# Performance work log

Hardware: AMD Instinct MI355X
Metric: run time of the kernel (lower is better)

The kernel has to match this reference:

```python
import jax, jax.numpy as jnp
import numpy as np

D_MODEL = 1024
D_HEAD = 64  # d_model / num_heads
NEG_INF = -1e9  # matches torch code's -1000000000.0 additive mask


def setup_inputs() -> dict:
    key = jax.random.key(0)
    ks = jax.random.split(key, 9)
    B, S = 4, 4096
    scale = 0.02
    return {
        "q": jax.random.normal(ks[0], (B, S, D_MODEL), dtype=jnp.float32),
        "k": jax.random.normal(ks[1], (B, S, D_MODEL), dtype=jnp.float32),
        "v": jax.random.normal(ks[2], (B, S, D_MODEL), dtype=jnp.float32),
        "WQ_w": jax.random.normal(ks[3], (D_HEAD, D_MODEL), dtype=jnp.float32) * scale,
        "WQ_b": jax.random.normal(ks[4], (D_HEAD,), dtype=jnp.float32) * scale,
        "WK_w": jax.random.normal(ks[5], (D_HEAD, D_MODEL), dtype=jnp.float32) * scale,
        "WK_b": jax.random.normal(ks[6], (D_HEAD,), dtype=jnp.float32) * scale,
        "WV_w": jax.random.normal(ks[7], (D_HEAD, D_MODEL), dtype=jnp.float32) * scale,
        "WV_b": jax.random.normal(ks[8], (D_HEAD,), dtype=jnp.float32) * scale,
    }


def reference(q, k, v, WQ_w, WQ_b, WK_w, WK_b, WV_w, WV_b):
    # Linear projections (torch nn.Linear: x @ W.T + b)
    qh = jnp.einsum("bsd,hd->bsh", q, WQ_w) + WQ_b  # [B,S,64]
    kh = jnp.einsum("bsd,hd->bsh", k, WK_w) + WK_b
    vh = jnp.einsum("bsd,hd->bsh", v, WV_w) + WV_b
    # Scaled dot-product scores [B,S,S]
    scores = jnp.einsum("bqh,bkh->bqk", qh, kh) / np.sqrt(D_HEAD).astype(np.float32)
    # Causal additive mask: upper triangle (j > i) gets -1e9
    S = scores.shape[-1]
    causal = jnp.triu(jnp.ones((S, S), dtype=scores.dtype), k=1) * NEG_INF
    scores = scores + causal
    attn = jax.nn.softmax(scores, axis=-1)
    out = jnp.einsum("bqk,bkh->bqh", attn, vh)  # [B,S,64]
    # Dropout is identity in eval mode (deterministic reference)
    return out
```

## Files before the change

### kernel.cpp

```cpp
#include <hip/hip_runtime.h>

#define SEQ 4096
#define DM  1024
#define DH  64
#define NB  4
#define SLOTS_PER_B 288

typedef __attribute__((ext_vector_type(4))) float  f32x4;
typedef __attribute__((ext_vector_type(8))) __bf16 bf16x8;

__device__ __forceinline__ unsigned short f2bf(float f) {
    unsigned int u = __float_as_uint(f);
    u += 0x7FFFu + ((u >> 16) & 1u);
    return (unsigned short)(u >> 16);
}

__device__ __forceinline__ unsigned short bfc(float f) {
    __bf16 h = (__bf16)f;
    return __builtin_bit_cast(unsigned short, h);
}

__device__ __forceinline__ bf16x8 cvt8(f32x4 lo, f32x4 hi) {
    bf16x8 r;
    r[0] = (__bf16)lo[0]; r[1] = (__bf16)lo[1]; r[2] = (__bf16)lo[2]; r[3] = (__bf16)lo[3];
    r[4] = (__bf16)hi[0]; r[5] = (__bf16)hi[1]; r[6] = (__bf16)hi[2]; r[7] = (__bf16)hi[3];
    return r;
}

__device__ __forceinline__ f32x4 mfma_bf16(bf16x8 a, bf16x8 b, f32x4 c) {
    return __builtin_amdgcn_mfma_f32_16x16x32_bf16(a, b, c, 0, 0, 0);
}

__global__ __launch_bounds__(256) void wprep_kernel(
    const float* __restrict__ Wq, const float* __restrict__ Wk, const float* __restrict__ Wv,
    unsigned short* __restrict__ Wf)
{
    const int which = blockIdx.y;
    const int kc    = blockIdx.x;
    const float* W  = (which == 0) ? Wq : (which == 1) ? Wk : Wv;
    unsigned short* out = Wf + (size_t)which * 65536 + (size_t)kc * 4096;
    const int t = threadIdx.x;
#pragma unroll
    for (int s = t; s < 512; s += 256) {
        const int ks = s >> 8, nt = (s >> 6) & 3, ln = s & 63;
        const int qd = ln >> 4, l = ln & 15;
        const float* src = W + (size_t)(nt * 16 + l) * DM + kc * 64 + ks * 32 + qd * 8;
        f32x4 v0 = *(const f32x4*)src;
        f32x4 v1 = *(const f32x4*)(src + 4);
        *(ushort4*)(out + (size_t)s * 8)     = make_ushort4(bfc(v0[0]), bfc(v0[1]), bfc(v0[2]), bfc(v0[3]));
        *(ushort4*)(out + (size_t)s * 8 + 4) = make_ushort4(bfc(v1[0]), bfc(v1[1]), bfc(v1[2]), bfc(v1[3]));
    }
}

__global__ __launch_bounds__(256) void proj_kernel(
    const float* __restrict__ xq, const float* __restrict__ xk, const float* __restrict__ xv,
    const unsigned short* __restrict__ Wf,
    const float* __restrict__ bq, const float* __restrict__ bk, const float* __restrict__ bv,
    unsigned short* __restrict__ qh, unsigned short* __restrict__ kh,
    unsigned short* __restrict__ vhT)
{
    __shared__ unsigned short ot[4][16][72];

    const int which = blockIdx.y;
    const float* X  = (which == 0) ? xq : (which == 1) ? xk : xv;
    const float* Bb = (which == 0) ? bq : (which == 1) ? bk : bv;
    const unsigned short* Wg = Wf + (size_t)which * 65536;

    const int m0   = blockIdx.x * 64;
    const int t    = threadIdx.x;
    const int wv   = t >> 6;
    const int lane = t & 63;
    const int quad = lane >> 4;
    const int l16  = lane & 15;

    const int row = m0 + wv * 16 + l16;
    const float* xrow = X + (size_t)row * DM + quad * 8;
    const unsigned short* wb = Wg + lane * 8;

    f32x4 acc[4];
#pragma unroll
    for (int i = 0; i < 4; ++i) acc[i] = f32x4{0.f, 0.f, 0.f, 0.f};

    f32x4 xa0 = *(const f32x4*)(xrow);
    f32x4 xa1 = *(const f32x4*)(xrow + 4);
    f32x4 xa2 = *(const f32x4*)(xrow + 32);
    f32x4 xa3 = *(const f32x4*)(xrow + 36);

#pragma unroll
    for (int kc = 0; kc < 16; ++kc) {
        bf16x8 b0 = *(const bf16x8*)(wb + (size_t)kc * 4096);
        bf16x8 b1 = *(const bf16x8*)(wb + (size_t)kc * 4096 + 512);
        bf16x8 b2 = *(const bf16x8*)(wb + (size_t)kc * 4096 + 1024);
        bf16x8 b3 = *(const bf16x8*)(wb + (size_t)kc * 4096 + 1536);
        bf16x8 b4 = *(const bf16x8*)(wb + (size_t)kc * 4096 + 2048);
        bf16x8 b5 = *(const bf16x8*)(wb + (size_t)kc * 4096 + 2560);
        bf16x8 b6 = *(const bf16x8*)(wb + (size_t)kc * 4096 + 3072);
        bf16x8 b7 = *(const bf16x8*)(wb + (size_t)kc * 4096 + 3584);

        f32x4 xn0, xn1, xn2, xn3;
        if (kc < 15) {
            const float* xp = xrow + (kc + 1) * 64;
            xn0 = *(const f32x4*)(xp);
            xn1 = *(const f32x4*)(xp + 4);
            xn2 = *(const f32x4*)(xp + 32);
            xn3 = *(const f32x4*)(xp + 36);
        }

        bf16x8 a0 = cvt8(xa0, xa1);
        bf16x8 a1 = cvt8(xa2, xa3);

        acc[0] = mfma_bf16(a0, b0, acc[0]);
        acc[1] = mfma_bf16(a0, b1, acc[1]);
        acc[2] = mfma_bf16(a0, b2, acc[2]);
        acc[3] = mfma_bf16(a0, b3, acc[3]);
        acc[0] = mfma_bf16(a1, b4, acc[0]);
        acc[1] = mfma_bf16(a1, b5, acc[1]);
        acc[2] = mfma_bf16(a1, b6, acc[2]);
        acc[3] = mfma_bf16(a1, b7, acc[3]);

        if (kc < 15) { xa0 = xn0; xa1 = xn1; xa2 = xn2; xa3 = xn3; }
    }

#pragma unroll
    for (int nt = 0; nt < 4; ++nt) {
        float bias = Bb[nt * 16 + l16];
#pragma unroll
        for (int r = 0; r < 4; ++r)
            ot[wv][quad * 4 + r][nt * 16 + l16] = f2bf(acc[nt][r] + bias);
    }
    asm volatile("s_waitcnt lgkmcnt(0)" ::: "memory");

    if (which < 2) {
        unsigned short* outp = (which == 0) ? qh : kh;
        const int r2 = lane >> 2;
        const int c2 = (lane & 3) << 4;
        unsigned short* og = outp + (size_t)(m0 + wv * 16 + r2) * DH + c2;
        *(int4*)og       = *(const int4*)&ot[wv][r2][c2];
        *(int4*)(og + 8) = *(const int4*)&ot[wv][r2][c2 + 8];
    } else {
        const int bb = m0 >> 12;
        const int s0 = (m0 & 4095) + wv * 16;
        __align__(16) unsigned short tmp[16];
#pragma unroll
        for (int i = 0; i < 16; ++i) tmp[i] = ot[wv][i][lane];
        unsigned short* og = vhT + (size_t)bb * DH * SEQ + (size_t)lane * SEQ + s0;
        *(int4*)og       = *(const int4*)&tmp[0];
        *(int4*)(og + 8) = *(const int4*)&tmp[8];
    }
}

__global__ __launch_bounds__(256) void attn_split_kernel(
    const unsigned short* __restrict__ qh, const unsigned short* __restrict__ kh,
    const unsigned short* __restrict__ vhT,
    float* __restrict__ pO, float* __restrict__ pm, float* __restrict__ pl)
{
    const int chunk = blockIdx.x;
    const int qt    = blockIdx.y;
    const int b     = blockIdx.z;
    const int nc    = (qt + 8) >> 3;
    if (chunk >= nc) return;

    const int g = qt >> 3, rr = qt & 7;
    const int slot = b * SLOTS_PER_B + 4 * g * (g + 1) + rr * (g + 1) + chunk;
    const int c0 = chunk * 8;
    const int c1 = min(c0 + 8, qt + 1);

    __shared__ unsigned short k_t[64][72];
    __shared__ unsigned short v_t[64][72];
    __shared__ unsigned short qp[64][72];

    const int t    = threadIdx.x;
    const int wv   = t >> 6;
    const int lane = t & 63;
    const int quad = lane >> 4;
    const int l16  = lane & 15;
    const int sr   = t >> 2;
    const int sc   = (t & 3) << 4;

    const size_t base = (size_t)b * SEQ * DH;

    {
        const unsigned short* gq = qh + base + (size_t)(qt * 64 + sr) * DH + sc;
        *(int4*)&qp[sr][sc]     = *(const int4*)gq;
        *(int4*)&qp[sr][sc + 8] = *(const int4*)(gq + 8);
    }
    __syncthreads();
    bf16x8 qfrag[2];
    qfrag[0] = *(const bf16x8*)&qp[wv * 16 + l16][quad * 8];
    qfrag[1] = *(const bf16x8*)&qp[wv * 16 + l16][32 + quad * 8];

    f32x4 o_acc[4];
#pragma unroll
    for (int i = 0; i < 4; ++i) o_acc[i] = f32x4{0.f, 0.f, 0.f, 0.f};
    float m_i[4], l_i[4];
#pragma unroll
    for (int r = 0; r < 4; ++r) { m_i[r] = -1e30f; l_i[r] = 0.f; }

    const int rowb = wv * 16 + quad * 4;

    for (int jt = c0; jt < c1; ++jt) {
        __syncthreads();
        {
            const unsigned short* kg = kh + base + (size_t)(jt * 64 + sr) * DH + sc;
            *(int4*)&k_t[sr][sc]     = *(const int4*)kg;
            *(int4*)&k_t[sr][sc + 8] = *(const int4*)(kg + 8);
            const unsigned short* vg = vhT + (size_t)b * DH * SEQ + (size_t)sr * SEQ + (jt * 64 + sc);
            *(int4*)&v_t[sr][sc]     = *(const int4*)vg;
            *(int4*)&v_t[sr][sc + 8] = *(const int4*)(vg + 8);
        }
        __syncthreads();

        f32x4 s_acc[4];
#pragma unroll
        for (int i = 0; i < 4; ++i) s_acc[i] = f32x4{0.f, 0.f, 0.f, 0.f};
#pragma unroll
        for (int ks = 0; ks < 2; ++ks) {
#pragma unroll
            for (int nt = 0; nt < 4; ++nt) {
                bf16x8 bfr = *(const bf16x8*)&k_t[nt * 16 + l16][ks * 32 + quad * 8];
                s_acc[nt] = mfma_bf16(qfrag[ks], bfr, s_acc[nt]);
            }
        }

        const bool diag = (jt == qt);
#pragma unroll
        for (int nt = 0; nt < 4; ++nt) {
            const int col = nt * 16 + l16;
#pragma unroll
            for (int r = 0; r < 4; ++r) {
                float sv = s_acc[nt][r] * 0.125f;
                if (diag && (col > rowb + r)) sv = -1e30f;
                s_acc[nt][r] = sv;
            }
        }

        float mx[4];
#pragma unroll
        for (int r = 0; r < 4; ++r)
            mx[r] = fmaxf(fmaxf(s_acc[0][r], s_acc[1][r]), fmaxf(s_acc[2][r], s_acc[3][r]));
#pragma unroll
        for (int off = 1; off < 16; off <<= 1)
#pragma unroll
            for (int r = 0; r < 4; ++r)
                mx[r] = fmaxf(mx[r], __shfl_xor(mx[r], off, 64));

        float alpha[4];
#pragma unroll
        for (int r = 0; r < 4; ++r) {
            float mn = fmaxf(m_i[r], mx[r]);
            alpha[r] = __expf(m_i[r] - mn);
            m_i[r]   = mn;
        }

        float rs[4] = {0.f, 0.f, 0.f, 0.f};
#pragma unroll
        for (int nt = 0; nt < 4; ++nt)
#pragma unroll
            for (int r = 0; r < 4; ++r) {
                float p = __expf(s_acc[nt][r] - m_i[r]);
                s_acc[nt][r] = p;
                rs[r] += p;
            }
#pragma unroll
        for (int off = 1; off < 16; off <<= 1)
#pragma unroll
            for (int r = 0; r < 4; ++r)
                rs[r] += __shfl_xor(rs[r], off, 64);
#pragma unroll
        for (int r = 0; r < 4; ++r) l_i[r] = l_i[r] * alpha[r] + rs[r];

#pragma unroll
        for (int nt = 0; nt < 4; ++nt)
#pragma unroll
            for (int r = 0; r < 4; ++r)
                qp[rowb + r][nt * 16 + l16] = f2bf(s_acc[nt][r]);

#pragma unroll
        for (int nt = 0; nt < 4; ++nt)
#pragma unroll
            for (int r = 0; r < 4; ++r)
                o_acc[nt][r] *= alpha[r];

#pragma unroll
        for (int ks = 0; ks < 2; ++ks) {
            bf16x8 pa = *(const bf16x8*)&qp[wv * 16 + l16][ks * 32 + quad * 8];
#pragma unroll
            for (int nt = 0; nt < 4; ++nt) {
                bf16x8 vb = *(const bf16x8*)&v_t[nt * 16 + l16][ks * 32 + quad * 8];
                o_acc[nt] = mfma_bf16(pa, vb, o_acc[nt]);
            }
        }
    }

    float* po = pO + (size_t)slot * 4096;
#pragma unroll
    for (int nt = 0; nt < 4; ++nt)
#pragma unroll
        for (int r = 0; r < 4; ++r)
            po[(rowb + r) * 64 + nt * 16 + l16] = o_acc[nt][r];
    if (l16 == 0) {
#pragma unroll
        for (int r = 0; r < 4; ++r) {
            pm[slot * 64 + rowb + r] = m_i[r];
            pl[slot * 64 + rowb + r] = l_i[r];
        }
    }
}

__global__ __launch_bounds__(256) void attn_merge_kernel(
    const float* __restrict__ pO, const float* __restrict__ pm, const float* __restrict__ pl,
    float* __restrict__ out)
{
    const int qt = blockIdx.x;
    const int b  = blockIdx.y;
    const int rq = blockIdx.z;
    const int nc = (qt + 8) >> 3;
    const int g = qt >> 3, rr = qt & 7;
    const int s0 = b * SLOTS_PER_B + 4 * g * (g + 1) + rr * (g + 1);

    const int t   = threadIdx.x;
    const int row = rq * 16 + (t >> 4);
    const int c0  = (t & 15) << 2;

    float mstar = -1e30f;
    for (int c = 0; c < nc; ++c)
        mstar = fmaxf(mstar, pm[(s0 + c) * 64 + row]);

    f32x4 acc = f32x4{0.f, 0.f, 0.f, 0.f};
    float lsum = 0.f;

    for (int c = 0; c < nc; ++c) {
        const float w = __expf(pm[(s0 + c) * 64 + row] - mstar);
        lsum += w * pl[(s0 + c) * 64 + row];
        f32x4 v = *(const f32x4*)(pO + (size_t)(s0 + c) * 4096 + row * 64 + c0);
        acc += w * v;
    }

    const float inv = 1.0f / lsum;
    float* og = out + (size_t)b * SEQ * DH + (size_t)(qt * 64 + row) * DH + c0;
    *(f32x4*)og = acc * inv;
}

extern "C" void kernel_launch(void* const* d_in, const int* in_sizes, int n_in,
                              void* d_out, int out_size, void* d_ws, size_t ws_size,
                              hipStream_t stream)
{
    (void)in_sizes; (void)n_in; (void)out_size; (void)ws_size;
    const float* q  = (const float*)d_in[0];
    const float* k  = (const float*)d_in[1];
    const float* v  = (const float*)d_in[2];
    const float* Wq = (const float*)d_in[3];
    const float* bq = (const float*)d_in[4];
    const float* Wk = (const float*)d_in[5];
    const float* bk = (const float*)d_in[6];
    const float* Wv = (const float*)d_in[7];
    const float* bv = (const float*)d_in[8];
    float* out = (float*)d_out;

    unsigned short* qh  = (unsigned short*)d_ws;
    unsigned short* kh  = qh + (size_t)NB * SEQ * DH;
    unsigned short* vhT = kh + (size_t)NB * SEQ * DH;
    float* pO = (float*)(vhT + (size_t)NB * SEQ * DH);
    float* pm = pO + (size_t)NB * SLOTS_PER_B * 4096;
    float* pl = pm + (size_t)NB * SLOTS_PER_B * 64;
    unsigned short* Wfb = (unsigned short*)pO;

    wprep_kernel<<<dim3(16, 3), 256, 0, stream>>>(Wq, Wk, Wv, Wfb);
    proj_kernel<<<dim3(NB * SEQ / 64, 3), 256, 0, stream>>>(
        q, k, v, Wfb, bq, bk, bv, qh, kh, vhT);
    attn_split_kernel<<<dim3(8, SEQ / 64, NB), 256, 0, stream>>>(qh, kh, vhT, pO, pm, pl);
    attn_merge_kernel<<<dim3(SEQ / 64, NB, 4), 256, 0, stream>>>(pO, pm, pl, out);
}
```

Measured before the change: 288.2 us.

## Split projection K dimension across waves with shared-memory reduction

The projection kernel now gives each block 16 rows instead of 64, and each of the 4 waves covers a quarter of the 1024-wide reduction. Partial sums are reduced through shared memory, and the bias and bf16 conversion are applied after the reduction. All of a wave's x loads are issued up front, which raises memory-level parallelism and gives the grid four times as many blocks for this bandwidth-bound stage. In exchange it adds a shared-memory reduction, extra barriers, more registers for the preloaded x values, and narrower 8-byte stores for vhT.

```diff
diff --git a/kernel.cpp b/kernel.cpp
--- a/kernel.cpp
+++ b/kernel.cpp
@@ -59,55 +59,51 @@
     unsigned short* __restrict__ qh, unsigned short* __restrict__ kh,
     unsigned short* __restrict__ vhT)
 {
-    __shared__ unsigned short ot[4][16][72];
+    __shared__ float red[4][16][68];
+    __shared__ unsigned short ot[16][68];
 
     const int which = blockIdx.y;
     const float* X  = (which == 0) ? xq : (which == 1) ? xk : xv;
     const float* Bb = (which == 0) ? bq : (which == 1) ? bk : bv;
     const unsigned short* Wg = Wf + (size_t)which * 65536;
 
-    const int m0   = blockIdx.x * 64;
+    const int m0   = blockIdx.x * 16;
     const int t    = threadIdx.x;
     const int wv   = t >> 6;
     const int lane = t & 63;
     const int quad = lane >> 4;
     const int l16  = lane & 15;
 
-    const int row = m0 + wv * 16 + l16;
-    const float* xrow = X + (size_t)row * DM + quad * 8;
+    const float* xrow = X + (size_t)(m0 + l16) * DM + wv * 256 + quad * 8;
     const unsigned short* wb = Wg + lane * 8;
 
+    f32x4 xa[16];
+#pragma unroll
+    for (int c = 0; c < 4; ++c) {
+        xa[c * 4 + 0] = *(const f32x4*)(xrow + c * 64);
+        xa[c * 4 + 1] = *(const f32x4*)(xrow + c * 64 + 4);
+        xa[c * 4 + 2] = *(const f32x4*)(xrow + c * 64 + 32);
+        xa[c * 4 + 3] = *(const f32x4*)(xrow + c * 64 + 36);
+    }
+
     f32x4 acc[4];
 #pragma unroll
     for (int i = 0; i < 4; ++i) acc[i] = f32x4{0.f, 0.f, 0.f, 0.f};
 
-    f32x4 xa0 = *(const f32x4*)(xrow);
-    f32x4 xa1 = *(const f32x4*)(xrow + 4);
-    f32x4 xa2 = *(const f32x4*)(xrow + 32);
-    f32x4 xa3 = *(const f32x4*)(xrow + 36);
-
-#pragma unroll
-    for (int kc = 0; kc < 16; ++kc) {
-        bf16x8 b0 = *(const bf16x8*)(wb + (size_t)kc * 4096);
-        bf16x8 b1 = *(const bf16x8*)(wb + (size_t)kc * 4096 + 512);
-        bf16x8 b2 = *(const bf16x8*)(wb + (size_t)kc * 4096 + 1024);
-        bf16x8 b3 = *(const bf16x8*)(wb + (size_t)kc * 4096 + 1536);
-        bf16x8 b4 = *(const bf16x8*)(wb + (size_t)kc * 4096 + 2048);
-        bf16x8 b5 = *(const bf16x8*)(wb + (size_t)kc * 4096 + 2560);
-        bf16x8 b6 = *(const bf16x8*)(wb + (size_t)kc * 4096 + 3072);
-        bf16x8 b7 = *(const bf16x8*)(wb + (size_t)kc * 4096 + 3584);
-
-        f32x4 xn0, xn1, xn2, xn3;
-        if (kc < 15) {
-            const float* xp = xrow + (kc + 1) * 64;
-            xn0 = *(const f32x4*)(xp);
-            xn1 = *(const f32x4*)(xp + 4);
-            xn2 = *(const f32x4*)(xp + 32);
-            xn3 = *(const f32x4*)(xp + 36);
-        }
-
-        bf16x8 a0 = cvt8(xa0, xa1);
-        bf16x8 a1 = cvt8(xa2, xa3);
+#pragma unroll
+    for (int c = 0; c < 4; ++c) {
+        const unsigned short* wc = wb + (size_t)(wv * 4 + c) * 4096;
+        bf16x8 b0 = *(const bf16x8*)(wc);
+        bf16x8 b1 = *(const bf16x8*)(wc + 512);
+        bf16x8 b2 = *(const bf16x8*)(wc + 1024);
+        bf16x8 b3 = *(const bf16x8*)(wc + 1536);
+        bf16x8 b4 = *(const bf16x8*)(wc + 2048);
+        bf16x8 b5 = *(const bf16x8*)(wc + 2560);
+        bf16x8 b6 = *(const bf16x8*)(wc + 3072);
+        bf16x8 b7 = *(const bf16x8*)(wc + 3584);
+
+        bf16x8 a0 = cvt8(xa[c * 4 + 0], xa[c * 4 + 1]);
+        bf16x8 a1 = cvt8(xa[c * 4 + 2], xa[c * 4 + 3]);
 
         acc[0] = mfma_bf16(a0, b0, acc[0]);
         acc[1] = mfma_bf16(a0, b1, acc[1]);
@@ -117,35 +113,41 @@
         acc[1] = mfma_bf16(a1, b5, acc[1]);
         acc[2] = mfma_bf16(a1, b6, acc[2]);
         acc[3] = mfma_bf16(a1, b7, acc[3]);
-
-        if (kc < 15) { xa0 = xn0; xa1 = xn1; xa2 = xn2; xa3 = xn3; }
-    }
-
-#pragma unroll
-    for (int nt = 0; nt < 4; ++nt) {
-        float bias = Bb[nt * 16 + l16];
+    }
+
+#pragma unroll
+    for (int nt = 0; nt < 4; ++nt)
 #pragma unroll
         for (int r = 0; r < 4; ++r)
-            ot[wv][quad * 4 + r][nt * 16 + l16] = f2bf(acc[nt][r] + bias);
-    }
-    asm volatile("s_waitcnt lgkmcnt(0)" ::: "memory");
+            red[wv][quad * 4 + r][nt * 16 + l16] = acc[nt][r];
+    __syncthreads();
+
+    const int row = t >> 4;
+    const int c0  = (t & 15) << 2;
+    f32x4 sum = *(const f32x4*)&red[0][row][c0];
+    sum += *(const f32x4*)&red[1][row][c0];
+    sum += *(const f32x4*)&red[2][row][c0];
+    sum += *(const f32x4*)&red[3][row][c0];
+    sum += *(const f32x4*)(Bb + c0);
 
     if (which < 2) {
         unsigned short* outp = (which == 0) ? qh : kh;
-        const int r2 = lane >> 2;
-        const int c2 = (lane & 3) << 4;
-        unsigned short* og = outp + (size_t)(m0 + wv * 16 + r2) * DH + c2;
-        *(int4*)og       = *(const int4*)&ot[wv][r2][c2];
-        *(int4*)(og + 8) = *(const int4*)&ot[wv][r2][c2 + 8];
+        unsigned short* og = outp + (size_t)(m0 + row) * DH + c0;
+        *(ushort4*)og = make_ushort4(f2bf(sum[0]), f2bf(sum[1]), f2bf(sum[2]), f2bf(sum[3]));
     } else {
+        ot[row][c0 + 0] = f2bf(sum[0]);
+        ot[row][c0 + 1] = f2bf(sum[1]);
+        ot[row][c0 + 2] = f2bf(sum[2]);
+        ot[row][c0 + 3] = f2bf(sum[3]);
+        __syncthreads();
+        const int h  = t & 63;
+        const int sq = t >> 6;
+        ushort4 o = make_ushort4(ot[sq * 4 + 0][h], ot[sq * 4 + 1][h],
+                                 ot[sq * 4 + 2][h], ot[sq * 4 + 3][h]);
         const int bb = m0 >> 12;
-        const int s0 = (m0 & 4095) + wv * 16;
-        __align__(16) unsigned short tmp[16];
-#pragma unroll
-        for (int i = 0; i < 16; ++i) tmp[i] = ot[wv][i][lane];
-        unsigned short* og = vhT + (size_t)bb * DH * SEQ + (size_t)lane * SEQ + s0;
-        *(int4*)og       = *(const int4*)&tmp[0];
-        *(int4*)(og + 8) = *(const int4*)&tmp[8];
+        const int s0 = (m0 & 4095) + sq * 4;
+        unsigned short* og = vhT + (size_t)bb * DH * SEQ + (size_t)h * SEQ + s0;
+        *(ushort4*)og = o;
     }
 }
 
@@ -366,7 +368,7 @@
     unsigned short* Wfb = (unsigned short*)pO;
 
     wprep_kernel<<<dim3(16, 3), 256, 0, stream>>>(Wq, Wk, Wv, Wfb);
-    proj_kernel<<<dim3(NB * SEQ / 64, 3), 256, 0, stream>>>(
+    proj_kernel<<<dim3(NB * SEQ / 16, 3), 256, 0, stream>>>(
         q, k, v, Wfb, bq, bk, bv, qh, kh, vhT);
     attn_split_kernel<<<dim3(8, SEQ / 64, NB), 256, 0, stream>>>(qh, kh, vhT, pO, pm, pl);
     attn_merge_kernel<<<dim3(SEQ / 64, NB, 4), 256, 0, stream>>>(pO, pm, pl, out);
```

Measured after the change: 282.8 us. No clear change (-1.9%).
